# Optimization experiments

Measured on AMD Instinct MI355X. Metric: run time of the kernel, lower is better.

The kernel has to match this reference:

```python
import jax, jax.numpy as jnp
import numpy as np
from jax import lax

INPUT_DIM = 64
HIDDEN = 128
NUM_CLASSES = 3


def _uniform(key, shape, scale):
    return jax.random.uniform(key, shape, jnp.float32, -scale, scale)


def setup_inputs() -> dict:
    key = jax.random.key(0)
    ks = jax.random.split(key, 16)
    s = 1.0 / np.sqrt(HIDDEN)
    inp = {
        "x": jax.random.normal(ks[0], (256, 512, INPUT_DIM), jnp.float32),
        # layer 0 LSTM params (PyTorch gate order: i, f, g, o)
        "W_ih0": _uniform(ks[1], (4 * HIDDEN, INPUT_DIM), s),
        "W_hh0": _uniform(ks[2], (4 * HIDDEN, HIDDEN), s),
        "b_ih0": _uniform(ks[3], (4 * HIDDEN,), s),
        "b_hh0": _uniform(ks[4], (4 * HIDDEN,), s),
        # layer 1 LSTM params
        "W_ih1": _uniform(ks[5], (4 * HIDDEN, HIDDEN), s),
        "W_hh1": _uniform(ks[6], (4 * HIDDEN, HIDDEN), s),
        "b_ih1": _uniform(ks[7], (4 * HIDDEN,), s),
        "b_hh1": _uniform(ks[8], (4 * HIDDEN,), s),
        # MLP head: fc1 (H -> H//2), fc2 (H//2 -> num_classes)
        "W1": _uniform(ks[9], (HIDDEN // 2, HIDDEN), s),
        "b1": _uniform(ks[10], (HIDDEN // 2,), s),
        "W2": _uniform(ks[11], (NUM_CLASSES, HIDDEN // 2), 1.0 / np.sqrt(HIDDEN // 2)),
        "b2": _uniform(ks[12], (NUM_CLASSES,), 1.0 / np.sqrt(HIDDEN // 2)),
    }
    return inp


def _lstm_layer(x, W_ih, W_hh, b_ih, b_hh):
    # x: [B, T, I] -> ys: [B, T, H]
    B = x.shape[0]
    H = W_hh.shape[1]
    b = b_ih + b_hh

    def step(carry, xt):
        h, c = carry
        g = xt @ W_ih.T + h @ W_hh.T + b  # [B, 4H]
        i, f, gg, o = jnp.split(g, 4, axis=-1)
        c = jax.nn.sigmoid(f) * c + jax.nn.sigmoid(i) * jnp.tanh(gg)
        h = jax.nn.sigmoid(o) * jnp.tanh(c)
        return (h, c), h

    h0 = jnp.zeros((B, H), x.dtype)
    (_, _), ys = lax.scan(step, (h0, h0), jnp.swapaxes(x, 0, 1))
    return jnp.swapaxes(ys, 0, 1)


def reference(x, W_ih0, W_hh0, b_ih0, b_hh0, W_ih1, W_hh1, b_ih1, b_hh1, W1, b1, W2, b2):
    # Eval mode: dropout layers are identity.
    h = _lstm_layer(x, W_ih0, W_hh0, b_ih0, b_hh0)   # [B, T, H]
    h = _lstm_layer(h, W_ih1, W_hh1, b_ih1, b_hh1)   # [B, T, H]
    last = h[:, -1, :]                                # [B, H]
    out = jax.nn.relu(last @ W1.T + b1) @ W2.T + b2   # [B, num_classes]
    return out
```

## Files before the change

kernel.cpp:

```cpp
#include <hip/hip_runtime.h>
#include <hip/hip_bf16.h>
#include <stdint.h>

#define BATCH 256
#define SEQ   512
#define INDIM 64
#define H     128
#define RB    4
#define NTILE 64
#define CH    16
#define NCH   (SEQ / CH)

#define WS_XB     0u
#define WS_H0RING 16777216u
#define WS_WB     20971520u
#define WS_BSUM   21430272u
#define WS_FLAGS  21434368u
#define WB_IH0 0
#define WB_HH0 32768
#define WB_IH1 98304
#define WB_HH1 163840
#define WB_TOT 229376

using short8  = __attribute__((ext_vector_type(8))) short;
using float4v = __attribute__((ext_vector_type(4))) float;

#define LOG2E 1.4426950408889634f

__device__ __forceinline__ unsigned short f2bf(float f) {
    union { float f; uint32_t u; } v; v.f = f;
    uint32_t u = v.u;
    return (unsigned short)((u + 0x7FFFu + ((u >> 16) & 1u)) >> 16);
}
__device__ __forceinline__ float fast_exp2(float x) {
#if __has_builtin(__builtin_amdgcn_exp2f)
    return __builtin_amdgcn_exp2f(x);
#else
    return __expf(x * 0.6931471805599453f);
#endif
}
__device__ __forceinline__ float fast_rcp(float x) {
#if __has_builtin(__builtin_amdgcn_rcpf)
    return __builtin_amdgcn_rcpf(x);
#else
    return 1.f / x;
#endif
}
__device__ __forceinline__ float sigmoid_fast(float x) {
    return fast_rcp(1.f + fast_exp2(-LOG2E * x));
}
__device__ __forceinline__ float tanh_fast(float x) {
    return fmaf(-2.f, fast_rcp(1.f + fast_exp2((2.f * LOG2E) * x)), 1.f);
}
__device__ __forceinline__ void light_barrier() {
    asm volatile("s_waitcnt lgkmcnt(0)\n\ts_barrier" ::: "memory");
}
__device__ __forceinline__ void spin_ge(const int* f, int target) {
    while (__hip_atomic_load(f, __ATOMIC_RELAXED, __HIP_MEMORY_SCOPE_AGENT) < target)
        __builtin_amdgcn_s_sleep(2);
    (void)__hip_atomic_load(f, __ATOMIC_ACQUIRE, __HIP_MEMORY_SCOPE_AGENT);
}
__device__ __forceinline__ void bump(int* f) {
    __hip_atomic_fetch_add(f, 1, __ATOMIC_RELEASE, __HIP_MEMORY_SCOPE_AGENT);
}

__global__ void conv_x_kernel(const float* __restrict__ x, unsigned short* __restrict__ xb) {
    int i = blockIdx.x * blockDim.x + threadIdx.x;
    float4 f = ((const float4*)x)[i];
    ushort4 o;
    o.x = f2bf(f.x); o.y = f2bf(f.y); o.z = f2bf(f.z); o.w = f2bf(f.w);
    ((ushort4*)xb)[i] = o;
}

__global__ void prep_w_kernel(const float* __restrict__ Wih0, const float* __restrict__ Whh0,
                              const float* __restrict__ Wih1, const float* __restrict__ Whh1,
                              const float* __restrict__ bih0, const float* __restrict__ bhh0,
                              const float* __restrict__ bih1, const float* __restrict__ bhh1,
                              unsigned short* __restrict__ wb, float* __restrict__ bsum,
                              int* __restrict__ flags) {
    int gid = blockIdx.x * blockDim.x + threadIdx.x;
    float v;
    if      (gid < WB_HH0) v = Wih0[gid];
    else if (gid < WB_IH1) v = Whh0[gid - WB_HH0];
    else if (gid < WB_HH1) v = Wih1[gid - WB_IH1];
    else                   v = Whh1[gid - WB_HH1];
    wb[gid] = f2bf(v);
    if (gid < 512)       bsum[gid] = bih0[gid] + bhh0[gid];
    else if (gid < 1024) bsum[gid] = bih1[gid - 512] + bhh1[gid - 512];
    if (gid < 128) flags[gid] = 0;
}

template<int KIN, bool IS_PROD>
__device__ __forceinline__ void lstm_block(
    const unsigned short* __restrict__ ain,
    const unsigned short* __restrict__ w_ih,
    const unsigned short* __restrict__ w_hh,
    const float* __restrict__ bsum,
    unsigned short* __restrict__ h0out,
    const float* __restrict__ W1, const float* __restrict__ b1,
    const float* __restrict__ W2, const float* __restrict__ b2,
    float* __restrict__ out,
    int* __restrict__ prodprog, int* __restrict__ consprog, int bt)
{
    constexpr int KT = KIN / 32;
    const int tid  = threadIdx.x;
    const int wave = tid >> 6, lane = tid & 63, quad = lane >> 4, l16 = lane & 15;
    const int b0   = bt * RB;

    __shared__ float gbuf[2][2][4][512];
    __shared__ short hbuf[2][16][132];
    __shared__ float hl[RB][128];
    __shared__ float mid[RB][65];

    if (wave < 8) {
        const int cell = wave * 16 + l16;
        const int arow = l16 & 12;
        for (int i = tid; i < 2 * 16 * 132; i += 512) ((short*)hbuf)[i] = 0;

        short8 whh_f[4][4];
#pragma unroll
        for (int tT = 0; tT < 4; tT++)
#pragma unroll
            for (int kt = 0; kt < 4; kt++)
                whh_f[tT][kt] = *(const short8*)(w_hh + (size_t)(tT * 128 + cell) * H + kt * 32 + quad * 8);

        if (!IS_PROD && tid == 0) spin_ge(prodprog, 2);
        __syncthreads();
        __syncthreads();
        float c0 = 0.f;

        auto rstep = [&](int CUR, int SB, unsigned short* hs, int i, bool last)
            __attribute__((always_inline)) {
            const float* gp = &gbuf[SB][CUR][0][tid];
            short8 ha0 = *(const short8*)&hbuf[CUR][arow][0 * 32 + quad * 8];
            short8 ha1 = *(const short8*)&hbuf[CUR][arow][1 * 32 + quad * 8];
            short8 ha2 = *(const short8*)&hbuf[CUR][arow][2 * 32 + quad * 8];
            short8 ha3 = *(const short8*)&hbuf[CUR][arow][3 * 32 + quad * 8];
            float4v a0 = (float4v){gp[0],    0.f, 0.f, 0.f};
            float4v a1 = (float4v){gp[512],  0.f, 0.f, 0.f};
            float4v a2 = (float4v){gp[1024], 0.f, 0.f, 0.f};
            float4v a3 = (float4v){gp[1536], 0.f, 0.f, 0.f};
            a0 = __builtin_amdgcn_mfma_f32_16x16x32_bf16(ha0, whh_f[0][0], a0, 0, 0, 0);
            a1 = __builtin_amdgcn_mfma_f32_16x16x32_bf16(ha0, whh_f[1][0], a1, 0, 0, 0);
            a2 = __builtin_amdgcn_mfma_f32_16x16x32_bf16(ha0, whh_f[2][0], a2, 0, 0, 0);
            a3 = __builtin_amdgcn_mfma_f32_16x16x32_bf16(ha0, whh_f[3][0], a3, 0, 0, 0);
            a0 = __builtin_amdgcn_mfma_f32_16x16x32_bf16(ha1, whh_f[0][1], a0, 0, 0, 0);
            a1 = __builtin_amdgcn_mfma_f32_16x16x32_bf16(ha1, whh_f[1][1], a1, 0, 0, 0);
            a2 = __builtin_amdgcn_mfma_f32_16x16x32_bf16(ha1, whh_f[2][1], a2, 0, 0, 0);
            a3 = __builtin_amdgcn_mfma_f32_16x16x32_bf16(ha1, whh_f[3][1], a3, 0, 0, 0);
            a0 = __builtin_amdgcn_mfma_f32_16x16x32_bf16(ha2, whh_f[0][2], a0, 0, 0, 0);
            a1 = __builtin_amdgcn_mfma_f32_16x16x32_bf16(ha2, whh_f[1][2], a1, 0, 0, 0);
            a2 = __builtin_amdgcn_mfma_f32_16x16x32_bf16(ha2, whh_f[2][2], a2, 0, 0, 0);
            a3 = __builtin_amdgcn_mfma_f32_16x16x32_bf16(ha2, whh_f[3][2], a3, 0, 0, 0);
            a0 = __builtin_amdgcn_mfma_f32_16x16x32_bf16(ha3, whh_f[0][3], a0, 0, 0, 0);
            a1 = __builtin_amdgcn_mfma_f32_16x16x32_bf16(ha3, whh_f[1][3], a1, 0, 0, 0);
            a2 = __builtin_amdgcn_mfma_f32_16x16x32_bf16(ha3, whh_f[2][3], a2, 0, 0, 0);
            a3 = __builtin_amdgcn_mfma_f32_16x16x32_bf16(ha3, whh_f[3][3], a3, 0, 0, 0);
            float si = sigmoid_fast(a0[0]);
            float sf = sigmoid_fast(a1[0]);
            float tg = tanh_fast(a2[0]);
            float so = sigmoid_fast(a3[0]);
            float cn = fmaf(sf, c0, si * tg);
            c0 = cn;
            float h = so * tanh_fast(cn);
            const unsigned short hb = f2bf(h);
            hbuf[CUR ^ 1][quad * 4][cell] = (short)hb;
            if (IS_PROD) {
                hs[(size_t)(i * 4 + quad) * H + cell] = hb;
            } else if (last) {
                hl[quad][cell] = h;
            }
            light_barrier();
        };

        for (int ch = 0; ch < NCH; ch++) {
            unsigned short* hs = IS_PROD ? h0out + (size_t)(ch & 3) * (64 * H) : nullptr;
            const bool lastCh = (ch == NCH - 1);
#pragma unroll 1
            for (int i = 0; i < CH; i += 4) {
                rstep(0, 0, hs, i + 0, false);
                rstep(1, 0, hs, i + 1, false);
                rstep(0, 1, hs, i + 2, false);
                rstep(1, 1, hs, i + 3, lastCh && (i + 3 == CH - 1));
            }
            __syncthreads();
            if (tid == 0) {
                bump(IS_PROD ? prodprog : consprog);
                if (ch + 1 < NCH) {
                    if (IS_PROD) { if (ch + 1 >= 4) spin_ge(consprog, ch - 2); }
                    else { int t = ch + 3 < NCH ? ch + 3 : NCH; spin_ge(prodprog, t); }
                }
            }
            __syncthreads();
        }
    } else {
        const int hw = wave - 8;
        short8 wih_f[4][KT];
        float  bias4[4];
#pragma unroll
        for (int j = 0; j < 4; j++) {
            const int n = hw * 64 + j * 16 + l16;
#pragma unroll
            for (int kt = 0; kt < KT; kt++)
                wih_f[j][kt] = *(const short8*)(w_ih + (size_t)n * KIN + kt * 32 + quad * 8);
            bias4[j] = bsum[n];
        }
        short8 af0[KT], af1[KT];
        const int m   = l16 & 7;
        const int ro  = m & 3;
        const int dio = m >> 2;

        auto loadA = [&](short8 (&af)[KT], int tw0) __attribute__((always_inline)) {
            const int t_tok = tw0 + dio;
            const unsigned short* ap;
            if (IS_PROD)
                ap = ain + ((size_t)(b0 + ro) * SEQ + t_tok) * KIN + quad * 8;
            else
                ap = ain + (size_t)((t_tok >> 4) & 3) * (64 * H)
                         + (size_t)((t_tok & 15) * 4 + ro) * H + quad * 8;
#pragma unroll
            for (int kt = 0; kt < KT; kt++) af[kt] = *(const short8*)(ap + kt * 32);
        };
        auto compWin = [&](short8 (&af)[KT], int SBD, int jA) __attribute__((always_inline)) {
#pragma unroll
            for (int jj = 0; jj < 2; jj++) {
                const int j  = jA + jj;
                const int cg = (hw * 4 + j) & 7;
                const int tT = (hw * 4 + j) >> 3;
                const float bs = bias4[j];
                float4v acc = (float4v){bs, bs, bs, bs};
#pragma unroll
                for (int kt = 0; kt < KT; kt++)
                    acc = __builtin_amdgcn_mfma_f32_16x16x32_bf16(af[kt], wih_f[j][kt], acc, 0, 0, 0);
                if (quad < 2) {
#pragma unroll
                    for (int reg = 0; reg < 4; reg++)
                        gbuf[SBD][quad][tT][cg * 64 + reg * 16 + l16] = acc[reg];
                }
            }
        };

        __syncthreads();
        loadA(af0, 0);
        compWin(af0, 0, 0);
        compWin(af0, 0, 2);
        loadA(af1, 2);
        __syncthreads();

        for (int ch = 0; ch < NCH; ch++) {
            const int tb = ch * CH;
#pragma unroll 1
            for (int i = 0; i < CH; i += 4) {
                const int t = tb + i;
                if (t <= 506) loadA(af0, t + 4);
                if (t <= 508) compWin(af1, 1, 0);
                light_barrier();
                if (t <= 508) compWin(af1, 1, 2);
                light_barrier();
                if (t <= 504) loadA(af1, t + 6);
                if (t <= 506) compWin(af0, 0, 0);
                light_barrier();
                if (t <= 506) compWin(af0, 0, 2);
                light_barrier();
            }
            __syncthreads();
            __syncthreads();
        }
    }

    if (!IS_PROD) {
        if (tid < RB * 64) {
            const int row = tid >> 6, j = tid & 63;
            float s = b1[j];
            const float* wr = W1 + (size_t)j * 128;
#pragma unroll 8
            for (int k = 0; k < 128; k++) s = fmaf(hl[row][k], wr[k], s);
            mid[row][j] = fmaxf(s, 0.f);
        }
        __syncthreads();
        if (tid < RB * 3) {
            const int row = tid / 3, k = tid - row * 3;
            float o = b2[k];
            const float* wr = W2 + (size_t)k * 64;
#pragma unroll 8
            for (int j = 0; j < 64; j++) o = fmaf(mid[row][j], wr[j], o);
            out[(size_t)(b0 + row) * 3 + k] = o;
        }
    }
}

__global__ __launch_bounds__(1024, 4)
void lstm_fused_kernel(const unsigned short* __restrict__ xb,
                       const unsigned short* __restrict__ wb,
                       const float* __restrict__ bsum,
                       unsigned short* __restrict__ h0ring,
                       const float* __restrict__ W1, const float* __restrict__ b1,
                       const float* __restrict__ W2, const float* __restrict__ b2,
                       float* __restrict__ out, int* __restrict__ flags)
{
    int* prodprog = flags;
    int* consprog = flags + 64;
    if (blockIdx.x < 64) {
        const int bt = blockIdx.x;
        lstm_block<64, true>(xb, wb + WB_IH0, wb + WB_HH0, bsum,
                             h0ring + (size_t)bt * (4 * 64 * H),
                             W1, b1, W2, b2, out,
                             &prodprog[bt], &consprog[bt], bt);
    } else {
        const int bt = blockIdx.x - 64;
        lstm_block<128, false>(h0ring + (size_t)bt * (4 * 64 * H),
                               wb + WB_IH1, wb + WB_HH1, bsum + 512,
                               nullptr,
                               W1, b1, W2, b2, out,
                               &prodprog[bt], &consprog[bt], bt);
    }
}

extern "C" void kernel_launch(void* const* d_in, const int* in_sizes, int n_in,
                              void* d_out, int out_size, void* d_ws, size_t ws_size,
                              hipStream_t stream) {
    const float* x     = (const float*)d_in[0];
    const float* W_ih0 = (const float*)d_in[1];
    const float* W_hh0 = (const float*)d_in[2];
    const float* b_ih0 = (const float*)d_in[3];
    const float* b_hh0 = (const float*)d_in[4];
    const float* W_ih1 = (const float*)d_in[5];
    const float* W_hh1 = (const float*)d_in[6];
    const float* b_ih1 = (const float*)d_in[7];
    const float* b_hh1 = (const float*)d_in[8];
    const float* W1    = (const float*)d_in[9];
    const float* b1    = (const float*)d_in[10];
    const float* W2    = (const float*)d_in[11];
    const float* b2    = (const float*)d_in[12];
    float* out = (float*)d_out;

    char* ws = (char*)d_ws;
    unsigned short* xb    = (unsigned short*)(ws + WS_XB);
    unsigned short* h0r   = (unsigned short*)(ws + WS_H0RING);
    unsigned short* wb    = (unsigned short*)(ws + WS_WB);
    float*          bsum  = (float*)(ws + WS_BSUM);
    int*            flags = (int*)(ws + WS_FLAGS);

    conv_x_kernel<<<8192, 256, 0, stream>>>(x, xb);
    prep_w_kernel<<<896, 256, 0, stream>>>(W_ih0, W_hh0, W_ih1, W_hh1,
                                           b_ih0, b_hh0, b_ih1, b_hh1, wb, bsum, flags);
    lstm_fused_kernel<<<128, 1024, 0, stream>>>(xb, wb, bsum, h0r,
                                                W1, b1, W2, b2, out, flags);
}
```

Before: 523.7 us.

## Process two interleaved batch tiles per block to hide recurrent step latency

Each workgroup now handles two independent 4-row batch tiles, halving the grid from 128 to 64 blocks. In each recurrent step the two tiles' MFMA chains and gate math are interleaved, so one tile's dependency latency can be covered by the other's work while sharing one barrier per step. Shared-memory gate buffers are relaid out so each thread reads its four gates as a single float4, and the input-projection waves alternate between the two tiles. The cost is twice the per-step work on a serial critical path and fewer active CUs.

```diff
diff --git a/kernel.cpp b/kernel.cpp
--- a/kernel.cpp
+++ b/kernel.cpp
@@ -7,9 +7,9 @@
 #define INDIM 64
 #define H     128
 #define RB    4
-#define NTILE 64
 #define CH    16
 #define NCH   (SEQ / CH)
+#define NBLK  32
 
 #define WS_XB     0u
 #define WS_H0RING 16777216u
@@ -63,6 +63,13 @@
 __device__ __forceinline__ void bump(int* f) {
     __hip_atomic_fetch_add(f, 1, __ATOMIC_RELEASE, __HIP_MEMORY_SCOPE_AGENT);
 }
+
+struct Smem {
+    float gbuf[2][2][2][512][4];
+    short hbuf[2][2][16][132];
+    float hl[8][128];
+    float mid[8][65];
+};
 
 __global__ void conv_x_kernel(const float* __restrict__ x, unsigned short* __restrict__ xb) {
     int i = blockIdx.x * blockDim.x + threadIdx.x;
@@ -92,30 +99,26 @@
 
 template<int KIN, bool IS_PROD>
 __device__ __forceinline__ void lstm_block(
-    const unsigned short* __restrict__ ain,
+    Smem* sm,
+    const unsigned short* __restrict__ xb,
+    unsigned short* __restrict__ hrA,
+    unsigned short* __restrict__ hrB,
     const unsigned short* __restrict__ w_ih,
     const unsigned short* __restrict__ w_hh,
     const float* __restrict__ bsum,
-    unsigned short* __restrict__ h0out,
     const float* __restrict__ W1, const float* __restrict__ b1,
     const float* __restrict__ W2, const float* __restrict__ b2,
     float* __restrict__ out,
-    int* __restrict__ prodprog, int* __restrict__ consprog, int bt)
+    int* __restrict__ prodprog, int* __restrict__ consprog, int btA)
 {
     constexpr int KT = KIN / 32;
     const int tid  = threadIdx.x;
     const int wave = tid >> 6, lane = tid & 63, quad = lane >> 4, l16 = lane & 15;
-    const int b0   = bt * RB;
-
-    __shared__ float gbuf[2][2][4][512];
-    __shared__ short hbuf[2][16][132];
-    __shared__ float hl[RB][128];
-    __shared__ float mid[RB][65];
 
     if (wave < 8) {
         const int cell = wave * 16 + l16;
         const int arow = l16 & 12;
-        for (int i = tid; i < 2 * 16 * 132; i += 512) ((short*)hbuf)[i] = 0;
+        for (int i = tid; i < 2 * 2 * 16 * 132; i += 512) ((short*)sm->hbuf)[i] = 0;
 
         short8 whh_f[4][4];
 #pragma unroll
@@ -127,61 +130,97 @@
         if (!IS_PROD && tid == 0) spin_ge(prodprog, 2);
         __syncthreads();
         __syncthreads();
-        float c0 = 0.f;
-
-        auto rstep = [&](int CUR, int SB, unsigned short* hs, int i, bool last)
-            __attribute__((always_inline)) {
-            const float* gp = &gbuf[SB][CUR][0][tid];
-            short8 ha0 = *(const short8*)&hbuf[CUR][arow][0 * 32 + quad * 8];
-            short8 ha1 = *(const short8*)&hbuf[CUR][arow][1 * 32 + quad * 8];
-            short8 ha2 = *(const short8*)&hbuf[CUR][arow][2 * 32 + quad * 8];
-            short8 ha3 = *(const short8*)&hbuf[CUR][arow][3 * 32 + quad * 8];
-            float4v a0 = (float4v){gp[0],    0.f, 0.f, 0.f};
-            float4v a1 = (float4v){gp[512],  0.f, 0.f, 0.f};
-            float4v a2 = (float4v){gp[1024], 0.f, 0.f, 0.f};
-            float4v a3 = (float4v){gp[1536], 0.f, 0.f, 0.f};
-            a0 = __builtin_amdgcn_mfma_f32_16x16x32_bf16(ha0, whh_f[0][0], a0, 0, 0, 0);
-            a1 = __builtin_amdgcn_mfma_f32_16x16x32_bf16(ha0, whh_f[1][0], a1, 0, 0, 0);
-            a2 = __builtin_amdgcn_mfma_f32_16x16x32_bf16(ha0, whh_f[2][0], a2, 0, 0, 0);
-            a3 = __builtin_amdgcn_mfma_f32_16x16x32_bf16(ha0, whh_f[3][0], a3, 0, 0, 0);
-            a0 = __builtin_amdgcn_mfma_f32_16x16x32_bf16(ha1, whh_f[0][1], a0, 0, 0, 0);
-            a1 = __builtin_amdgcn_mfma_f32_16x16x32_bf16(ha1, whh_f[1][1], a1, 0, 0, 0);
-            a2 = __builtin_amdgcn_mfma_f32_16x16x32_bf16(ha1, whh_f[2][1], a2, 0, 0, 0);
-            a3 = __builtin_amdgcn_mfma_f32_16x16x32_bf16(ha1, whh_f[3][1], a3, 0, 0, 0);
-            a0 = __builtin_amdgcn_mfma_f32_16x16x32_bf16(ha2, whh_f[0][2], a0, 0, 0, 0);
-            a1 = __builtin_amdgcn_mfma_f32_16x16x32_bf16(ha2, whh_f[1][2], a1, 0, 0, 0);
-            a2 = __builtin_amdgcn_mfma_f32_16x16x32_bf16(ha2, whh_f[2][2], a2, 0, 0, 0);
-            a3 = __builtin_amdgcn_mfma_f32_16x16x32_bf16(ha2, whh_f[3][2], a3, 0, 0, 0);
-            a0 = __builtin_amdgcn_mfma_f32_16x16x32_bf16(ha3, whh_f[0][3], a0, 0, 0, 0);
-            a1 = __builtin_amdgcn_mfma_f32_16x16x32_bf16(ha3, whh_f[1][3], a1, 0, 0, 0);
-            a2 = __builtin_amdgcn_mfma_f32_16x16x32_bf16(ha3, whh_f[2][3], a2, 0, 0, 0);
-            a3 = __builtin_amdgcn_mfma_f32_16x16x32_bf16(ha3, whh_f[3][3], a3, 0, 0, 0);
-            float si = sigmoid_fast(a0[0]);
-            float sf = sigmoid_fast(a1[0]);
-            float tg = tanh_fast(a2[0]);
-            float so = sigmoid_fast(a3[0]);
-            float cn = fmaf(sf, c0, si * tg);
-            c0 = cn;
-            float h = so * tanh_fast(cn);
-            const unsigned short hb = f2bf(h);
-            hbuf[CUR ^ 1][quad * 4][cell] = (short)hb;
-            if (IS_PROD) {
-                hs[(size_t)(i * 4 + quad) * H + cell] = hb;
-            } else if (last) {
-                hl[quad][cell] = h;
+        float cA = 0.f, cB = 0.f;
+
+        auto rstep = [&](int CUR, int SB, unsigned short* hsA, unsigned short* hsB,
+                         int i, bool last) __attribute__((always_inline)) {
+            short8 h0 = *(const short8*)&sm->hbuf[0][CUR][arow][0 * 32 + quad * 8];
+            short8 h1 = *(const short8*)&sm->hbuf[0][CUR][arow][1 * 32 + quad * 8];
+            short8 h2 = *(const short8*)&sm->hbuf[0][CUR][arow][2 * 32 + quad * 8];
+            short8 h3 = *(const short8*)&sm->hbuf[0][CUR][arow][3 * 32 + quad * 8];
+            float4 giA = *(const float4*)&sm->gbuf[0][SB][CUR][tid][0];
+            float4v a0 = (float4v){giA.x, 0.f, 0.f, 0.f};
+            float4v a1 = (float4v){giA.y, 0.f, 0.f, 0.f};
+            float4v a2 = (float4v){giA.z, 0.f, 0.f, 0.f};
+            float4v a3 = (float4v){giA.w, 0.f, 0.f, 0.f};
+            a0 = __builtin_amdgcn_mfma_f32_16x16x32_bf16(h0, whh_f[0][0], a0, 0, 0, 0);
+            a1 = __builtin_amdgcn_mfma_f32_16x16x32_bf16(h0, whh_f[1][0], a1, 0, 0, 0);
+            a2 = __builtin_amdgcn_mfma_f32_16x16x32_bf16(h0, whh_f[2][0], a2, 0, 0, 0);
+            a3 = __builtin_amdgcn_mfma_f32_16x16x32_bf16(h0, whh_f[3][0], a3, 0, 0, 0);
+            a0 = __builtin_amdgcn_mfma_f32_16x16x32_bf16(h1, whh_f[0][1], a0, 0, 0, 0);
+            a1 = __builtin_amdgcn_mfma_f32_16x16x32_bf16(h1, whh_f[1][1], a1, 0, 0, 0);
+            a2 = __builtin_amdgcn_mfma_f32_16x16x32_bf16(h1, whh_f[2][1], a2, 0, 0, 0);
+            a3 = __builtin_amdgcn_mfma_f32_16x16x32_bf16(h1, whh_f[3][1], a3, 0, 0, 0);
+            a0 = __builtin_amdgcn_mfma_f32_16x16x32_bf16(h2, whh_f[0][2], a0, 0, 0, 0);
+            a1 = __builtin_amdgcn_mfma_f32_16x16x32_bf16(h2, whh_f[1][2], a1, 0, 0, 0);
+            a2 = __builtin_amdgcn_mfma_f32_16x16x32_bf16(h2, whh_f[2][2], a2, 0, 0, 0);
+            a3 = __builtin_amdgcn_mfma_f32_16x16x32_bf16(h2, whh_f[3][2], a3, 0, 0, 0);
+            a0 = __builtin_amdgcn_mfma_f32_16x16x32_bf16(h3, whh_f[0][3], a0, 0, 0, 0);
+            a1 = __builtin_amdgcn_mfma_f32_16x16x32_bf16(h3, whh_f[1][3], a1, 0, 0, 0);
+            a2 = __builtin_amdgcn_mfma_f32_16x16x32_bf16(h3, whh_f[2][3], a2, 0, 0, 0);
+            a3 = __builtin_amdgcn_mfma_f32_16x16x32_bf16(h3, whh_f[3][3], a3, 0, 0, 0);
+            float gA0 = a0[0], gA1 = a1[0], gA2 = a2[0], gA3 = a3[0];
+            short8 k0 = *(const short8*)&sm->hbuf[1][CUR][arow][0 * 32 + quad * 8];
+            short8 k1 = *(const short8*)&sm->hbuf[1][CUR][arow][1 * 32 + quad * 8];
+            short8 k2 = *(const short8*)&sm->hbuf[1][CUR][arow][2 * 32 + quad * 8];
+            short8 k3 = *(const short8*)&sm->hbuf[1][CUR][arow][3 * 32 + quad * 8];
+            float4 giB = *(const float4*)&sm->gbuf[1][SB][CUR][tid][0];
+            float4v c0v = (float4v){giB.x, 0.f, 0.f, 0.f};
+            float4v c1v = (float4v){giB.y, 0.f, 0.f, 0.f};
+            float4v c2v = (float4v){giB.z, 0.f, 0.f, 0.f};
+            float4v c3v = (float4v){giB.w, 0.f, 0.f, 0.f};
+            c0v = __builtin_amdgcn_mfma_f32_16x16x32_bf16(k0, whh_f[0][0], c0v, 0, 0, 0);
+            c1v = __builtin_amdgcn_mfma_f32_16x16x32_bf16(k0, whh_f[1][0], c1v, 0, 0, 0);
+            c2v = __builtin_amdgcn_mfma_f32_16x16x32_bf16(k0, whh_f[2][0], c2v, 0, 0, 0);
+            c3v = __builtin_amdgcn_mfma_f32_16x16x32_bf16(k0, whh_f[3][0], c3v, 0, 0, 0);
+            c0v = __builtin_amdgcn_mfma_f32_16x16x32_bf16(k1, whh_f[0][1], c0v, 0, 0, 0);
+            c1v = __builtin_amdgcn_mfma_f32_16x16x32_bf16(k1, whh_f[1][1], c1v, 0, 0, 0);
+            c2v = __builtin_amdgcn_mfma_f32_16x16x32_bf16(k1, whh_f[2][1], c2v, 0, 0, 0);
+            c3v = __builtin_amdgcn_mfma_f32_16x16x32_bf16(k1, whh_f[3][1], c3v, 0, 0, 0);
+            c0v = __builtin_amdgcn_mfma_f32_16x16x32_bf16(k2, whh_f[0][2], c0v, 0, 0, 0);
+            c1v = __builtin_amdgcn_mfma_f32_16x16x32_bf16(k2, whh_f[1][2], c1v, 0, 0, 0);
+            c2v = __builtin_amdgcn_mfma_f32_16x16x32_bf16(k2, whh_f[2][2], c2v, 0, 0, 0);
+            c3v = __builtin_amdgcn_mfma_f32_16x16x32_bf16(k2, whh_f[3][2], c3v, 0, 0, 0);
+            c0v = __builtin_amdgcn_mfma_f32_16x16x32_bf16(k3, whh_f[0][3], c0v, 0, 0, 0);
+            c1v = __builtin_amdgcn_mfma_f32_16x16x32_bf16(k3, whh_f[1][3], c1v, 0, 0, 0);
+            c2v = __builtin_amdgcn_mfma_f32_16x16x32_bf16(k3, whh_f[2][3], c2v, 0, 0, 0);
+            c3v = __builtin_amdgcn_mfma_f32_16x16x32_bf16(k3, whh_f[3][3], c3v, 0, 0, 0);
+            float gB0 = c0v[0], gB1 = c1v[0], gB2 = c2v[0], gB3 = c3v[0];
+            {
+                float si = sigmoid_fast(gA0), sf = sigmoid_fast(gA1);
+                float tg = tanh_fast(gA2),   so = sigmoid_fast(gA3);
+                float cn = fmaf(sf, cA, si * tg);
+                cA = cn;
+                float h = so * tanh_fast(cn);
+                const unsigned short hbv = f2bf(h);
+                sm->hbuf[0][CUR ^ 1][quad * 4][cell] = (short)hbv;
+                if (IS_PROD) hsA[(size_t)(i * 4 + quad) * H + cell] = hbv;
+                else if (last) sm->hl[quad][cell] = h;
+            }
+            {
+                float si = sigmoid_fast(gB0), sf = sigmoid_fast(gB1);
+                float tg = tanh_fast(gB2),   so = sigmoid_fast(gB3);
+                float cn = fmaf(sf, cB, si * tg);
+                cB = cn;
+                float h = so * tanh_fast(cn);
+                const unsigned short hbv = f2bf(h);
+                sm->hbuf[1][CUR ^ 1][quad * 4][cell] = (short)hbv;
+                if (IS_PROD) hsB[(size_t)(i * 4 + quad) * H + cell] = hbv;
+                else if (last) sm->hl[4 + quad][cell] = h;
             }
             light_barrier();
         };
 
         for (int ch = 0; ch < NCH; ch++) {
-            unsigned short* hs = IS_PROD ? h0out + (size_t)(ch & 3) * (64 * H) : nullptr;
+            unsigned short* hsA = IS_PROD ? hrA + (size_t)(ch & 3) * (64 * H) : nullptr;
+            unsigned short* hsB = IS_PROD ? hrB + (size_t)(ch & 3) * (64 * H) : nullptr;
             const bool lastCh = (ch == NCH - 1);
 #pragma unroll 1
             for (int i = 0; i < CH; i += 4) {
-                rstep(0, 0, hs, i + 0, false);
-                rstep(1, 0, hs, i + 1, false);
-                rstep(0, 1, hs, i + 2, false);
-                rstep(1, 1, hs, i + 3, lastCh && (i + 3 == CH - 1));
+                rstep(0, 0, hsA, hsB, i + 0, false);
+                rstep(1, 0, hsA, hsB, i + 1, false);
+                rstep(0, 1, hsA, hsB, i + 2, false);
+                rstep(1, 1, hsA, hsB, i + 3, lastCh && (i + 3 == CH - 1));
             }
             __syncthreads();
             if (tid == 0) {
@@ -195,6 +234,7 @@
         }
     } else {
         const int hw = wave - 8;
+        const int b0A = btA * RB, b0B = b0A + RB;
         short8 wih_f[4][KT];
         float  bias4[4];
 #pragma unroll
@@ -205,28 +245,24 @@
                 wih_f[j][kt] = *(const short8*)(w_ih + (size_t)n * KIN + kt * 32 + quad * 8);
             bias4[j] = bsum[n];
         }
-        short8 af0[KT], af1[KT];
-        const int m   = l16 & 7;
-        const int ro  = m & 3;
-        const int dio = m >> 2;
-
-        auto loadA = [&](short8 (&af)[KT], int tw0) __attribute__((always_inline)) {
+        const int m = l16 & 7, ro = m & 3, dio = m >> 2;
+
+        auto loadAfrag = [&](short8 (&af)[KT], const unsigned short* ring, int b0r, int tw0)
+            __attribute__((always_inline)) {
             const int t_tok = tw0 + dio;
             const unsigned short* ap;
             if (IS_PROD)
-                ap = ain + ((size_t)(b0 + ro) * SEQ + t_tok) * KIN + quad * 8;
+                ap = xb + ((size_t)(b0r + ro) * SEQ + t_tok) * KIN + quad * 8;
             else
-                ap = ain + (size_t)((t_tok >> 4) & 3) * (64 * H)
-                         + (size_t)((t_tok & 15) * 4 + ro) * H + quad * 8;
+                ap = ring + (size_t)((t_tok >> 4) & 3) * (64 * H)
+                          + (size_t)((t_tok & 15) * 4 + ro) * H + quad * 8;
 #pragma unroll
             for (int kt = 0; kt < KT; kt++) af[kt] = *(const short8*)(ap + kt * 32);
         };
-        auto compWin = [&](short8 (&af)[KT], int SBD, int jA) __attribute__((always_inline)) {
-#pragma unroll
-            for (int jj = 0; jj < 2; jj++) {
-                const int j  = jA + jj;
-                const int cg = (hw * 4 + j) & 7;
-                const int tT = (hw * 4 + j) >> 3;
+        auto compWin = [&](short8 (&af)[KT], int TILE, int SBD) __attribute__((always_inline)) {
+#pragma unroll
+            for (int j = 0; j < 4; j++) {
+                const int cg = (hw * 4 + j) & 7, tT = (hw * 4 + j) >> 3;
                 const float bs = bias4[j];
                 float4v acc = (float4v){bs, bs, bs, bs};
 #pragma unroll
@@ -235,32 +271,35 @@
                 if (quad < 2) {
 #pragma unroll
                     for (int reg = 0; reg < 4; reg++)
-                        gbuf[SBD][quad][tT][cg * 64 + reg * 16 + l16] = acc[reg];
+                        sm->gbuf[TILE][SBD][quad][cg * 64 + reg * 16 + l16][tT] = acc[reg];
                 }
             }
         };
 
-        __syncthreads();
-        loadA(af0, 0);
-        compWin(af0, 0, 0);
-        compWin(af0, 0, 2);
-        loadA(af1, 2);
+        short8 afA[KT], afB[KT];
+        __syncthreads();
+        loadAfrag(afA, hrA, b0A, 0); compWin(afA, 0, 0);
+        loadAfrag(afB, hrB, b0B, 0); compWin(afB, 1, 0);
+        loadAfrag(afA, hrA, b0A, 2);
+        loadAfrag(afB, hrB, b0B, 2);
         __syncthreads();
 
         for (int ch = 0; ch < NCH; ch++) {
-            const int tb = ch * CH;
+            const int r0 = ch * CH;
 #pragma unroll 1
             for (int i = 0; i < CH; i += 4) {
-                const int t = tb + i;
-                if (t <= 506) loadA(af0, t + 4);
-                if (t <= 508) compWin(af1, 1, 0);
+                const int r = r0 + i;
+                if (r + 2 < SEQ) compWin(afA, 0, 1);
+                if (r + 4 < SEQ) loadAfrag(afA, hrA, b0A, r + 4);
                 light_barrier();
-                if (t <= 508) compWin(af1, 1, 2);
+                if (r + 3 < SEQ) compWin(afB, 1, 1);
+                if (r + 5 < SEQ) loadAfrag(afB, hrB, b0B, r + 4);
                 light_barrier();
-                if (t <= 504) loadA(af1, t + 6);
-                if (t <= 506) compWin(af0, 0, 0);
+                if (r + 4 < SEQ) compWin(afA, 0, 0);
+                if (r + 6 < SEQ) loadAfrag(afA, hrA, b0A, r + 6);
                 light_barrier();
-                if (t <= 506) compWin(af0, 0, 2);
+                if (r + 5 < SEQ) compWin(afB, 1, 0);
+                if (r + 7 < SEQ) loadAfrag(afB, hrB, b0B, r + 6);
                 light_barrier();
             }
             __syncthreads();
@@ -269,27 +308,27 @@
     }
 
     if (!IS_PROD) {
-        if (tid < RB * 64) {
+        if (tid < 512) {
             const int row = tid >> 6, j = tid & 63;
             float s = b1[j];
             const float* wr = W1 + (size_t)j * 128;
 #pragma unroll 8
-            for (int k = 0; k < 128; k++) s = fmaf(hl[row][k], wr[k], s);
-            mid[row][j] = fmaxf(s, 0.f);
-        }
-        __syncthreads();
-        if (tid < RB * 3) {
+            for (int k = 0; k < 128; k++) s = fmaf(sm->hl[row][k], wr[k], s);
+            sm->mid[row][j] = fmaxf(s, 0.f);
+        }
+        __syncthreads();
+        if (tid < 24) {
             const int row = tid / 3, k = tid - row * 3;
             float o = b2[k];
             const float* wr = W2 + (size_t)k * 64;
 #pragma unroll 8
-            for (int j = 0; j < 64; j++) o = fmaf(mid[row][j], wr[j], o);
-            out[(size_t)(b0 + row) * 3 + k] = o;
+            for (int j = 0; j < 64; j++) o = fmaf(sm->mid[row][j], wr[j], o);
+            out[(size_t)(btA * RB + row) * 3 + k] = o;
         }
     }
 }
 
-__global__ __launch_bounds__(1024, 4)
+__global__ __launch_bounds__(1024)
 void lstm_fused_kernel(const unsigned short* __restrict__ xb,
                        const unsigned short* __restrict__ wb,
                        const float* __restrict__ bsum,
@@ -298,21 +337,25 @@
                        const float* __restrict__ W2, const float* __restrict__ b2,
                        float* __restrict__ out, int* __restrict__ flags)
 {
+    __shared__ Smem sm;
     int* prodprog = flags;
-    int* consprog = flags + 64;
-    if (blockIdx.x < 64) {
-        const int bt = blockIdx.x;
-        lstm_block<64, true>(xb, wb + WB_IH0, wb + WB_HH0, bsum,
-                             h0ring + (size_t)bt * (4 * 64 * H),
+    int* consprog = flags + NBLK;
+    if (blockIdx.x < NBLK) {
+        const int bid = blockIdx.x;
+        lstm_block<64, true>(&sm, xb,
+                             h0ring + (size_t)(2 * bid) * (4 * 64 * H),
+                             h0ring + (size_t)(2 * bid + 1) * (4 * 64 * H),
+                             wb + WB_IH0, wb + WB_HH0, bsum,
                              W1, b1, W2, b2, out,
-                             &prodprog[bt], &consprog[bt], bt);
+                             &prodprog[bid], &consprog[bid], 2 * bid);
     } else {
-        const int bt = blockIdx.x - 64;
-        lstm_block<128, false>(h0ring + (size_t)bt * (4 * 64 * H),
+        const int bid = blockIdx.x - NBLK;
+        lstm_block<128, false>(&sm, xb,
+                               h0ring + (size_t)(2 * bid) * (4 * 64 * H),
+                               h0ring + (size_t)(2 * bid + 1) * (4 * 64 * H),
                                wb + WB_IH1, wb + WB_HH1, bsum + 512,
-                               nullptr,
                                W1, b1, W2, b2, out,
-                               &prodprog[bt], &consprog[bt], bt);
+                               &prodprog[bid], &consprog[bid], 2 * bid);
     }
 }
 
@@ -344,6 +387,6 @@
     conv_x_kernel<<<8192, 256, 0, stream>>>(x, xb);
     prep_w_kernel<<<896, 256, 0, stream>>>(W_ih0, W_hh0, W_ih1, W_hh1,
                                            b_ih0, b_hh0, b_ih1, b_hh1, wb, bsum, flags);
-    lstm_fused_kernel<<<128, 1024, 0, stream>>>(xb, wb, bsum, h0r,
-                                                W1, b1, W2, b2, out, flags);
-}
+    lstm_fused_kernel<<<2 * NBLK, 1024, 0, stream>>>(xb, wb, bsum, h0r,
+                                                     W1, b1, W2, b2, out, flags);
+}
```

Result: slower. 1.042 ms (+99.0%).
